# Kernel tuning notes

Measured on AMD Instinct MI355X. Metric: run time of the kernel, lower is better.

The kernel has to match this reference:

```python
import jax, jax.numpy as jnp
import numpy as np

BN_EPS = 1e-5


def setup_inputs() -> dict:
    key = jax.random.key(0)
    ks = jax.random.split(key, 7)
    B, C, N = 8, 512, 2048
    P = C // 2
    x = jax.random.normal(ks[0], (B, C, N), dtype=jnp.float32)
    # 1x1 conv weights (no bias), shape [out, in]
    Wg = jax.random.normal(ks[1], (P, C), dtype=jnp.float32) * (1.0 / np.sqrt(C))
    Wtheta = jax.random.normal(ks[2], (P, C), dtype=jnp.float32) * (1.0 / np.sqrt(C))
    Wphi = jax.random.normal(ks[3], (P, C), dtype=jnp.float32) * (1.0 / np.sqrt(C))
    Wz = jax.random.normal(ks[4], (C, P), dtype=jnp.float32) * (1.0 / np.sqrt(P))
    gamma = jnp.ones((C,), dtype=jnp.float32)
    beta = jnp.zeros((C,), dtype=jnp.float32)
    return {"x": x, "Wg": Wg, "Wtheta": Wtheta, "Wphi": Wphi, "Wz": Wz,
            "gamma": gamma, "beta": beta}


def reference(x, Wg, Wtheta, Wphi, Wz, gamma, beta):
    # x: [B, C, N]
    g = jnp.einsum('pc,bcn->bnp', Wg, x)        # [B, N, P]
    theta = jnp.einsum('pc,bcn->bnp', Wtheta, x)  # [B, N, P]
    phi = jnp.einsum('pc,bcn->bpn', Wphi, x)      # [B, P, N]
    f = jnp.einsum('bnp,bpm->bnm', theta, phi)    # [B, N, N] unscaled scores
    f = jax.nn.softmax(f, axis=-1)
    y = jnp.einsum('bnm,bmp->bpn', f, g)          # [B, P, N]
    z = jnp.einsum('cp,bpn->bcn', Wz, y)          # [B, C, N]
    # BatchNorm1d (training-mode batch stats over batch and length dims)
    mean = jnp.mean(z, axis=(0, 2), keepdims=True)
    var = jnp.mean((z - mean) ** 2, axis=(0, 2), keepdims=True)
    z_bn = (z - mean) / jnp.sqrt(var + BN_EPS)
    z_bn = z_bn * gamma[None, :, None] + beta[None, :, None]
    return z_bn + x
```

## Files before the change

### kernel.cpp

```cpp
#include <hip/hip_runtime.h>
#include <hip/hip_bf16.h>


typedef __attribute__((ext_vector_type(8))) short short8;
typedef __attribute__((ext_vector_type(4))) float floatx4;

__device__ __forceinline__ unsigned short f2bf(float v) {
    __hip_bfloat16 h = __float2bfloat16(v);
    return *(unsigned short*)&h;
}
__device__ __forceinline__ float bf2f(unsigned short u) {
    __hip_bfloat16 h;
    *(unsigned short*)&h = u;
    return __bfloat162float(h);
}

__global__ __launch_bounds__(256) void transpose_split(
    const float* __restrict__ X, unsigned short* __restrict__ Thi,
    unsigned short* __restrict__ Tlo, int R, int N)
{
    X   += (long)blockIdx.z * R * N;
    Thi += (long)blockIdx.z * N * R;
    Tlo += (long)blockIdx.z * N * R;
    __shared__ float s[32][33];
    const int tx = threadIdx.x & 31, ty = threadIdx.x >> 5;
    const int n0 = blockIdx.x * 32, r0 = blockIdx.y * 32;
#pragma unroll
    for (int r = 0; r < 4; ++r)
        s[ty + r * 8][tx] = X[(long)(r0 + ty + r * 8) * N + n0 + tx];
    __syncthreads();
#pragma unroll
    for (int r = 0; r < 4; ++r) {
        const int n = ty + r * 8;
        const float v = s[tx][n];
        const unsigned short hi = f2bf(v);
        const unsigned short lo = f2bf(v - bf2f(hi));
        Thi[(long)(n0 + n) * R + r0 + tx] = hi;
        Tlo[(long)(n0 + n) * R + r0 + tx] = lo;
    }
}

__global__ __launch_bounds__(256) void split_w2(
    const float* __restrict__ Wth, const float* __restrict__ Wph,
    unsigned short* __restrict__ Whi, unsigned short* __restrict__ Wlo, int PC)
{
    const int i = blockIdx.x * 256 + threadIdx.x;
    if (i < 2 * PC) {
        const float v = (i < PC) ? Wth[i] : Wph[i - PC];
        const unsigned short hi = f2bf(v);
        Whi[i] = hi;
        Wlo[i] = f2bf(v - bf2f(hi));
    }
}

__global__ __launch_bounds__(256) void cast_bf16(
    const float* __restrict__ X, unsigned short* __restrict__ Y)
{
    const long i = ((long)blockIdx.x * 256 + threadIdx.x) * 4;
    const float4 v = *(const float4*)&X[i];
    ushort4 o;
    o.x = f2bf(v.x); o.y = f2bf(v.y); o.z = f2bf(v.z); o.w = f2bf(v.w);
    *(ushort4*)&Y[i] = o;
}

#define BK 32

template <bool SPLIT, int OUTMODE, int FM, int FN>
__global__ __launch_bounds__(256) void mfma_gemm(
    const unsigned short* __restrict__ Ahi, const unsigned short* __restrict__ Alo,
    const unsigned short* __restrict__ Bhi, const unsigned short* __restrict__ Blo,
    void* __restrict__ Cout, void* __restrict__ Cout2,
    int K, int lda, int ldb, int ldc,
    long sA, long sB, long sC,
    float* __restrict__ S1, float* __restrict__ S2)
{
    constexpr int MTM = FM * 32, MTN = FN * 32;
    constexpr int SA = FM / 2, SB = FN / 2;

    Ahi += (long)blockIdx.z * sA;
    Bhi += (long)blockIdx.z * sB;
    if (SPLIT) { Alo += (long)blockIdx.z * sA; Blo += (long)blockIdx.z * sB; }
    float* Cf = (float*)Cout + (long)blockIdx.z * sC;
    unsigned short* Ch = (unsigned short*)Cout + (long)blockIdx.z * sC;
    unsigned short* Cl = (unsigned short*)Cout2 + (long)blockIdx.z * sC;

    __shared__ unsigned short AsH[MTM * BK], BsH[MTN * BK];
    __shared__ unsigned short AsL[SPLIT ? MTM * BK : 8], BsL[SPLIT ? MTN * BK : 8];

    const int tid = threadIdx.x;
    const int wid = tid >> 6, lane = tid & 63;
    const int wm = (wid >> 1) * (FM * 16), wn = (wid & 1) * (FN * 16);
    const int l15 = lane & 15, quad = lane >> 4;
    const int m0 = blockIdx.y * MTM, n0 = blockIdx.x * MTN;

    int arow[SA], acol[SA], brow[SB], bcol[SB];
#pragma unroll
    for (int t = 0; t < SA; ++t) {
        const int gid = t * 256 + tid;
        arow[t] = gid >> 2; acol[t] = (gid & 3) * 8;
    }
#pragma unroll
    for (int t = 0; t < SB; ++t) {
        const int gid = t * 256 + tid;
        brow[t] = gid >> 2; bcol[t] = (gid & 3) * 8;
    }

    short8 pa[SA], pb[SB], paL[SPLIT ? SA : 1], pbL[SPLIT ? SB : 1];

    auto loadTiles = [&](int k0) {
#pragma unroll
        for (int t = 0; t < SA; ++t) {
            const long o = (long)(m0 + arow[t]) * lda + k0 + acol[t];
            pa[t] = *(const short8*)&Ahi[o];
            if (SPLIT) paL[t] = *(const short8*)&Alo[o];
        }
#pragma unroll
        for (int t = 0; t < SB; ++t) {
            const long o = (long)(n0 + brow[t]) * ldb + k0 + bcol[t];
            pb[t] = *(const short8*)&Bhi[o];
            if (SPLIT) pbL[t] = *(const short8*)&Blo[o];
        }
    };
    auto writeTiles = [&]() {
#pragma unroll
        for (int t = 0; t < SA; ++t) {
            *(short8*)&AsH[arow[t] * BK + acol[t]] = pa[t];
            if (SPLIT) *(short8*)&AsL[arow[t] * BK + acol[t]] = paL[t];
        }
#pragma unroll
        for (int t = 0; t < SB; ++t) {
            *(short8*)&BsH[brow[t] * BK + bcol[t]] = pb[t];
            if (SPLIT) *(short8*)&BsL[brow[t] * BK + bcol[t]] = pbL[t];
        }
    };

    floatx4 acc[FM][FN];
#pragma unroll
    for (int i = 0; i < FM; ++i)
#pragma unroll
        for (int j = 0; j < FN; ++j) acc[i][j] = (floatx4){0.f, 0.f, 0.f, 0.f};

    const int iters = K / BK;
    loadTiles(0);
    writeTiles();
    __syncthreads();

    for (int it = 0; it < iters; ++it) {
        if (it + 1 < iters) loadTiles((it + 1) * BK);

        short8 ah[FM], bh[FN], al[SPLIT ? FM : 1], bl[SPLIT ? FN : 1];
#pragma unroll
        for (int i = 0; i < FM; ++i) {
            ah[i] = *(const short8*)&AsH[(wm + i * 16 + l15) * BK + quad * 8];
            if (SPLIT) al[i] = *(const short8*)&AsL[(wm + i * 16 + l15) * BK + quad * 8];
        }
#pragma unroll
        for (int j = 0; j < FN; ++j) {
            bh[j] = *(const short8*)&BsH[(wn + j * 16 + l15) * BK + quad * 8];
            if (SPLIT) bl[j] = *(const short8*)&BsL[(wn + j * 16 + l15) * BK + quad * 8];
        }
#pragma unroll
        for (int i = 0; i < FM; ++i)
#pragma unroll
            for (int j = 0; j < FN; ++j) {
                acc[i][j] = __builtin_amdgcn_mfma_f32_16x16x32_bf16(ah[i], bh[j], acc[i][j], 0, 0, 0);
                if (SPLIT) {
                    acc[i][j] = __builtin_amdgcn_mfma_f32_16x16x32_bf16(ah[i], bl[j], acc[i][j], 0, 0, 0);
                    acc[i][j] = __builtin_amdgcn_mfma_f32_16x16x32_bf16(al[i], bh[j], acc[i][j], 0, 0, 0);
                }
            }

        if (it + 1 < iters) {
            __syncthreads();
            writeTiles();
            __syncthreads();
        }
    }

#pragma unroll
    for (int i = 0; i < FM; ++i)
#pragma unroll
        for (int j = 0; j < FN; ++j) {
            const int m = m0 + wm + i * 16 + quad * 4;
            const int n = n0 + wn + j * 16 + l15;
#pragma unroll
            for (int r = 0; r < 4; ++r) {
                const float v = acc[i][j][r];
                const long idx = (long)(m + r) * ldc + n;
                if (OUTMODE == 0) {
                    Cf[idx] = v;
                } else if (OUTMODE == 1 || OUTMODE == 3) {
                    Ch[idx] = f2bf(v);
                } else {
                    const unsigned short hi = f2bf(v);
                    Ch[idx] = hi;
                    Cl[idx] = f2bf(v - bf2f(hi));
                }
            }
        }

    if (OUTMODE == 3) {
        const int slot = (blockIdx.z * gridDim.x + blockIdx.x) * 2 + (wn >> 6);
#pragma unroll
        for (int i = 0; i < FM; ++i)
#pragma unroll
            for (int r = 0; r < 4; ++r) {
                float s = 0.f, q = 0.f;
#pragma unroll
                for (int j = 0; j < FN; ++j) {
                    const float v = acc[i][j][r];
                    s += v; q += v * v;
                }
#pragma unroll
                for (int msk = 1; msk < 16; msk <<= 1) {
                    s += __shfl_xor(s, msk, 64);
                    q += __shfl_xor(q, msk, 64);
                }
                if (l15 == 0) {
                    const int row = m0 + wm + i * 16 + quad * 4 + r;
                    S1[(long)row * 256 + slot] = s;
                    S2[(long)row * 256 + slot] = q;
                }
            }
    }
}

#define FSTR 72
#define GSTR 72
#define PSTRP 136

__global__ __launch_bounds__(256) void fused_attn(
    const unsigned short* __restrict__ thphH,
    const unsigned short* __restrict__ thphL,
    const unsigned short* __restrict__ gbf,
    unsigned short* __restrict__ ybf)
{
    const int N = 2048, P = 256, P2 = 512;
    const int id = blockIdx.x;
    const int b  = id & 7;
    const int qt = id >> 3;
    const int q0 = qt * 64;

    const unsigned short* thB = thphH + (long)b * N * P2;
    const unsigned short* tlB = thphL + (long)b * N * P2;
    const unsigned short* gB  = gbf   + (long)b * P * N;
    unsigned short*       yB  = ybf   + (long)b * N * P;

    __shared__ unsigned short Fh[128 * FSTR], Fl[128 * FSTR];
    __shared__ unsigned short Gs[256 * GSTR];
    __shared__ unsigned short Pw[4][16 * PSTRP];

    const int tid = threadIdx.x;
    const int wid = tid >> 6, lane = tid & 63;
    const int l15 = lane & 15, quad = lane >> 4;

    short8 tHr[8], tLr[8];
    {
        const unsigned short* t1 = thB + (long)(q0 + wid * 16 + l15) * P2;
        const unsigned short* t2 = tlB + (long)(q0 + wid * 16 + l15) * P2;
#pragma unroll
        for (int kt = 0; kt < 8; ++kt) {
            tHr[kt] = *(const short8*)&t1[kt * 32 + quad * 8];
            tLr[kt] = *(const short8*)&t2[kt * 32 + quad * 8];
        }
    }

    float mrun[4], lrun[4];
#pragma unroll
    for (int r = 0; r < 4; ++r) { mrun[r] = -1e30f; lrun[r] = 0.f; }

    floatx4 oacc[16];
#pragma unroll
    for (int p = 0; p < 16; ++p) oacc[p] = (floatx4){0.f, 0.f, 0.f, 0.f};

    const int prow = tid >> 3, pc8 = (tid & 7) * 8;
    short8 pfH[4], pfL[4], pg[8];

    auto loadPhi = [&](int m0, int kc) {
#pragma unroll
        for (int s = 0; s < 4; ++s) {
            const long o = (long)(m0 + prow + s * 32) * P2 + P + kc * 64 + pc8;
            pfH[s] = *(const short8*)&thB[o];
            pfL[s] = *(const short8*)&tlB[o];
        }
    };
    auto writePhi = [&]() {
#pragma unroll
        for (int s = 0; s < 4; ++s) {
            *(short8*)&Fh[(prow + s * 32) * FSTR + pc8] = pfH[s];
            *(short8*)&Fl[(prow + s * 32) * FSTR + pc8] = pfL[s];
        }
    };
    auto loadG = [&](int m0, int mc) {
#pragma unroll
        for (int s = 0; s < 8; ++s)
            pg[s] = *(const short8*)&gB[(long)(prow + s * 32) * N + m0 + mc * 64 + pc8];
    };
    auto writeG = [&]() {
#pragma unroll
        for (int s = 0; s < 8; ++s)
            *(short8*)&Gs[(prow + s * 32) * GSTR + pc8] = pg[s];
    };

    for (int mt = 0; mt < 16; ++mt) {
        const int m0 = mt * 128;

        floatx4 sacc[8];
#pragma unroll
        for (int j = 0; j < 8; ++j) sacc[j] = (floatx4){0.f, 0.f, 0.f, 0.f};

        loadPhi(m0, 0);
        writePhi();
        __syncthreads();
#pragma unroll
        for (int kc = 0; kc < 4; ++kc) {
            if (kc < 3) loadPhi(m0, kc + 1);
#pragma unroll
            for (int ks = 0; ks < 2; ++ks) {
                const short8 aH = tHr[kc * 2 + ks];
                const short8 aL = tLr[kc * 2 + ks];
#pragma unroll
                for (int j = 0; j < 8; ++j) {
                    const int ro = (j * 16 + l15) * FSTR + ks * 32 + quad * 8;
                    const short8 bh = *(const short8*)&Fh[ro];
                    const short8 bl = *(const short8*)&Fl[ro];
                    sacc[j] = __builtin_amdgcn_mfma_f32_16x16x32_bf16(aH, bh, sacc[j], 0, 0, 0);
                    sacc[j] = __builtin_amdgcn_mfma_f32_16x16x32_bf16(aH, bl, sacc[j], 0, 0, 0);
                    sacc[j] = __builtin_amdgcn_mfma_f32_16x16x32_bf16(aL, bh, sacc[j], 0, 0, 0);
                }
            }
            if (kc < 3) {
                __syncthreads();
                writePhi();
                __syncthreads();
            }
        }

        float alpha[4];
#pragma unroll
        for (int r = 0; r < 4; ++r) {
            float v = sacc[0][r];
#pragma unroll
            for (int j = 1; j < 8; ++j) v = fmaxf(v, sacc[j][r]);
            v = fmaxf(v, __shfl_xor(v, 1, 64));
            v = fmaxf(v, __shfl_xor(v, 2, 64));
            v = fmaxf(v, __shfl_xor(v, 4, 64));
            v = fmaxf(v, __shfl_xor(v, 8, 64));
            const float mo = mrun[r];
            const float mn = fmaxf(mo, v);
            mrun[r] = mn;
            alpha[r] = __expf(mo - mn);
        }
        float lpart[4] = {0.f, 0.f, 0.f, 0.f};
#pragma unroll
        for (int j = 0; j < 8; ++j)
#pragma unroll
            for (int r = 0; r < 4; ++r) {
                const float p = __expf(sacc[j][r] - mrun[r]);
                Pw[wid][(quad * 4 + r) * PSTRP + j * 16 + l15] = f2bf(p);
                lpart[r] += p;
            }
#pragma unroll
        for (int r = 0; r < 4; ++r) {
            float s = lpart[r];
            s += __shfl_xor(s, 1, 64);
            s += __shfl_xor(s, 2, 64);
            s += __shfl_xor(s, 4, 64);
            s += __shfl_xor(s, 8, 64);
            lrun[r] = lrun[r] * alpha[r] + s;
        }
#pragma unroll
        for (int p = 0; p < 16; ++p)
#pragma unroll
            for (int r = 0; r < 4; ++r) oacc[p][r] *= alpha[r];

        loadG(m0, 0);
        writeG();
        __syncthreads();
#pragma unroll
        for (int mc = 0; mc < 2; ++mc) {
            if (mc == 0) loadG(m0, 1);
#pragma unroll
            for (int kk = 0; kk < 2; ++kk) {
                const short8 af = *(const short8*)&Pw[wid][l15 * PSTRP + mc * 64 + kk * 32 + quad * 8];
#pragma unroll
                for (int pj = 0; pj < 16; ++pj) {
                    const short8 bg = *(const short8*)&Gs[(pj * 16 + l15) * GSTR + kk * 32 + quad * 8];
                    oacc[pj] = __builtin_amdgcn_mfma_f32_16x16x32_bf16(af, bg, oacc[pj], 0, 0, 0);
                }
            }
            if (mc == 0) {
                __syncthreads();
                writeG();
                __syncthreads();
            }
        }
    }

    float linv[4];
#pragma unroll
    for (int r = 0; r < 4; ++r) linv[r] = 1.0f / lrun[r];
#pragma unroll
    for (int pj = 0; pj < 16; ++pj)
#pragma unroll
        for (int r = 0; r < 4; ++r) {
            const int row = q0 + wid * 16 + quad * 4 + r;
            const int col = pj * 16 + l15;
            yB[(long)row * P + col] = f2bf(oacc[pj][r] * linv[r]);
        }
}

__global__ __launch_bounds__(256) void bn_finalize(
    const float* __restrict__ p1, const float* __restrict__ p2,
    float* __restrict__ mean, float* __restrict__ rstd, float cnt)
{
    const int c = blockIdx.x, t = threadIdx.x;
    __shared__ float rs[256], rq[256];
    rs[t] = p1[(long)c * 256 + t];
    rq[t] = p2[(long)c * 256 + t];
    __syncthreads();
    for (int st = 128; st > 0; st >>= 1) {
        if (t < st) { rs[t] += rs[t + st]; rq[t] += rq[t + st]; }
        __syncthreads();
    }
    if (t == 0) {
        const float m = rs[0] / cnt;
        mean[c] = m;
        rstd[c] = rsqrtf(rq[0] / cnt - m * m + 1e-5f);
    }
}

__global__ __launch_bounds__(256) void bn_apply_bf(
    const unsigned short* __restrict__ z, const float* __restrict__ x,
    const float* __restrict__ mean, const float* __restrict__ rstd,
    const float* __restrict__ gamma, const float* __restrict__ beta,
    float* __restrict__ out, int C, int N)
{
    const long i = ((long)blockIdx.x * 256 + threadIdx.x) * 8;
    const int c = (int)((i / N) % C);
    const float mu = mean[c], rs = rstd[c], ga = gamma[c], be = beta[c];
    const ushort4 z0 = *(const ushort4*)&z[i];
    const ushort4 z1 = *(const ushort4*)&z[i + 4];
    const float4 x0 = *(const float4*)&x[i];
    const float4 x1 = *(const float4*)&x[i + 4];
    float4 o0, o1;
    o0.x = (bf2f(z0.x) - mu) * rs * ga + be + x0.x;
    o0.y = (bf2f(z0.y) - mu) * rs * ga + be + x0.y;
    o0.z = (bf2f(z0.z) - mu) * rs * ga + be + x0.z;
    o0.w = (bf2f(z0.w) - mu) * rs * ga + be + x0.w;
    o1.x = (bf2f(z1.x) - mu) * rs * ga + be + x1.x;
    o1.y = (bf2f(z1.y) - mu) * rs * ga + be + x1.y;
    o1.z = (bf2f(z1.z) - mu) * rs * ga + be + x1.z;
    o1.w = (bf2f(z1.w) - mu) * rs * ga + be + x1.w;
    *(float4*)&out[i] = o0;
    *(float4*)&out[i + 4] = o1;
}

extern "C" void kernel_launch(void* const* d_in, const int* in_sizes, int n_in,
                              void* d_out, int out_size, void* d_ws, size_t ws_size,
                              hipStream_t stream)
{
    const int B = 8, C = 512, N = 2048, P = 256;
    const float* x      = (const float*)d_in[0];
    const float* Wg     = (const float*)d_in[1];
    const float* Wtheta = (const float*)d_in[2];
    const float* Wphi   = (const float*)d_in[3];
    const float* Wz     = (const float*)d_in[4];
    const float* gamma  = (const float*)d_in[5];
    const float* beta   = (const float*)d_in[6];
    float* out = (float*)d_out;

    float* ws = (float*)d_ws;
    const long NCle = (long)N * C;
    const long NP   = (long)N * P;
    const long R0   = (long)B * NCle;
    unsigned short* xtH   = (unsigned short*)ws;
    unsigned short* xtL   = xtH + B * NCle;
    unsigned short* zbf   = (unsigned short*)ws;
    unsigned short* thphH = (unsigned short*)(ws + R0);
    unsigned short* thphL = thphH + B * NCle;
    unsigned short* gbf   = (unsigned short*)(ws + 2 * R0);
    unsigned short* fbf   = gbf + B * NP;
    unsigned short* ybf   = fbf + (long)B * N * N;
    unsigned short* W2H   = ybf + B * NP;
    unsigned short* W2L   = W2H + 2L * P * C;
    unsigned short* WgB   = W2L + 2L * P * C;
    unsigned short* WzB   = WgB + (long)P * C;
    float*          bnp1  = ws + R0;
    float*          bnp2  = bnp1 + (long)C * 256;
    float*          mean  = bnp2 + (long)C * 256;
    float*          rstd  = mean + C;

    const long sX = (long)C * N;
    const int  P2 = 2 * P;

    transpose_split<<<dim3(N / 32, C / 32, B), 256, 0, stream>>>(x, xtH, xtL, C, N);
    split_w2<<<(2 * P * C + 255) / 256, 256, 0, stream>>>(Wtheta, Wphi, W2H, W2L, P * C);
    cast_bf16<<<P * C / 1024, 256, 0, stream>>>(Wg, WgB);
    cast_bf16<<<P * C / 1024, 256, 0, stream>>>(Wz, WzB);

    mfma_gemm<true, 2, 4, 4><<<dim3(P2 / 128, N / 128, B), 256, 0, stream>>>(
        xtH, xtL, W2H, W2L, thphH, thphL, C, C, C, P2, NCle, 0, NCle, nullptr, nullptr);
    mfma_gemm<false, 1, 2, 4><<<dim3(N / 128, P / 64, B), 256, 0, stream>>>(
        WgB, WgB, xtH, xtH, gbf, gbf, C, C, C, N, 0, NCle, NP, nullptr, nullptr);

    fused_attn<<<dim3(256), 256, 0, stream>>>(thphH, thphL, gbf, ybf);

    mfma_gemm<false, 3, 4, 4><<<dim3(N / 128, C / 128, B), 256, 0, stream>>>(
        WzB, WzB, ybf, ybf, zbf, zbf, P, P, P, N, 0, NP, sX, bnp1, bnp2);

    bn_finalize<<<C, 256, 0, stream>>>(bnp1, bnp2, mean, rstd, (float)B * N);
    bn_apply_bf<<<(int)((B * sX) / 2048), 256, 0, stream>>>(zbf, x, mean, rstd, gamma, beta, out, C, N);
}
```

Baseline: 297.4 us.

## Split attention key range across two blocks and merge partial softmax results

The fused attention kernel now splits the key dimension into two halves, launching 512 blocks instead of 256. Each block writes unnormalized fp32 partial outputs plus running max and sum, and a new merge kernel rescales and combines them into the bf16 y tensor. This aims to fill more compute units on a GPU with many CUs, where 256 blocks underutilize the device. In exchange it adds fp32 partial-output traffic and an extra launch. The phi staging tile is also narrowed to 32 columns per chunk with a smaller LDS stride, which means more sync rounds per tile.

```diff
diff --git a/kernel.cpp b/kernel.cpp
--- a/kernel.cpp
+++ b/kernel.cpp
@@ -225,7 +225,7 @@
     }
 }
 
-#define FSTR 72
+#define FSTR4 40
 #define GSTR 72
 #define PSTRP 136
 
@@ -233,20 +233,26 @@
     const unsigned short* __restrict__ thphH,
     const unsigned short* __restrict__ thphL,
     const unsigned short* __restrict__ gbf,
-    unsigned short* __restrict__ ybf)
+    float* __restrict__ Opart,
+    float* __restrict__ Mpart,
+    float* __restrict__ Lpart)
 {
     const int N = 2048, P = 256, P2 = 512;
+    const long BN = 8L * 2048;
     const int id = blockIdx.x;
-    const int b  = id & 7;
-    const int qt = id >> 3;
+    const int b    = id & 7;
+    const int qt   = (id >> 3) & 31;
+    const int half = id >> 8;
     const int q0 = qt * 64;
 
     const unsigned short* thB = thphH + (long)b * N * P2;
     const unsigned short* tlB = thphL + (long)b * N * P2;
     const unsigned short* gB  = gbf   + (long)b * P * N;
-    unsigned short*       yB  = ybf   + (long)b * N * P;
-
-    __shared__ unsigned short Fh[128 * FSTR], Fl[128 * FSTR];
+    float* Oh = Opart + (long)half * BN * P;
+    float* Mh = Mpart + (long)half * BN;
+    float* Lh = Lpart + (long)half * BN;
+
+    __shared__ unsigned short Fh[128 * FSTR4], Fl[128 * FSTR4];
     __shared__ unsigned short Gs[256 * GSTR];
     __shared__ unsigned short Pw[4][16 * PSTRP];
 
@@ -273,36 +279,39 @@
 #pragma unroll
     for (int p = 0; p < 16; ++p) oacc[p] = (floatx4){0.f, 0.f, 0.f, 0.f};
 
-    const int prow = tid >> 3, pc8 = (tid & 7) * 8;
-    short8 pfH[4], pfL[4], pg[8];
+    short8 pfH[2], pfL[2], pg[8];
+    const int grow = tid >> 3, gc8 = (tid & 7) * 8;
 
     auto loadPhi = [&](int m0, int kc) {
 #pragma unroll
-        for (int s = 0; s < 4; ++s) {
-            const long o = (long)(m0 + prow + s * 32) * P2 + P + kc * 64 + pc8;
+        for (int s = 0; s < 2; ++s) {
+            const int gid = s * 256 + tid;
+            const long o = (long)(m0 + (gid >> 2)) * P2 + P + kc * 32 + (gid & 3) * 8;
             pfH[s] = *(const short8*)&thB[o];
             pfL[s] = *(const short8*)&tlB[o];
         }
     };
     auto writePhi = [&]() {
 #pragma unroll
-        for (int s = 0; s < 4; ++s) {
-            *(short8*)&Fh[(prow + s * 32) * FSTR + pc8] = pfH[s];
-            *(short8*)&Fl[(prow + s * 32) * FSTR + pc8] = pfL[s];
+        for (int s = 0; s < 2; ++s) {
+            const int gid = s * 256 + tid;
+            const int lo = (gid >> 2) * FSTR4 + (gid & 3) * 8;
+            *(short8*)&Fh[lo] = pfH[s];
+            *(short8*)&Fl[lo] = pfL[s];
         }
     };
     auto loadG = [&](int m0, int mc) {
 #pragma unroll
         for (int s = 0; s < 8; ++s)
-            pg[s] = *(const short8*)&gB[(long)(prow + s * 32) * N + m0 + mc * 64 + pc8];
+            pg[s] = *(const short8*)&gB[(long)(grow + s * 32) * N + m0 + mc * 64 + gc8];
     };
     auto writeG = [&]() {
 #pragma unroll
         for (int s = 0; s < 8; ++s)
-            *(short8*)&Gs[(prow + s * 32) * GSTR + pc8] = pg[s];
+            *(short8*)&Gs[(grow + s * 32) * GSTR + gc8] = pg[s];
     };
 
-    for (int mt = 0; mt < 16; ++mt) {
+    for (int mt = half * 8; mt < half * 8 + 8; ++mt) {
         const int m0 = mt * 128;
 
         floatx4 sacc[8];
@@ -313,23 +322,20 @@
         writePhi();
         __syncthreads();
 #pragma unroll
-        for (int kc = 0; kc < 4; ++kc) {
-            if (kc < 3) loadPhi(m0, kc + 1);
-#pragma unroll
-            for (int ks = 0; ks < 2; ++ks) {
-                const short8 aH = tHr[kc * 2 + ks];
-                const short8 aL = tLr[kc * 2 + ks];
-#pragma unroll
-                for (int j = 0; j < 8; ++j) {
-                    const int ro = (j * 16 + l15) * FSTR + ks * 32 + quad * 8;
-                    const short8 bh = *(const short8*)&Fh[ro];
-                    const short8 bl = *(const short8*)&Fl[ro];
-                    sacc[j] = __builtin_amdgcn_mfma_f32_16x16x32_bf16(aH, bh, sacc[j], 0, 0, 0);
-                    sacc[j] = __builtin_amdgcn_mfma_f32_16x16x32_bf16(aH, bl, sacc[j], 0, 0, 0);
-                    sacc[j] = __builtin_amdgcn_mfma_f32_16x16x32_bf16(aL, bh, sacc[j], 0, 0, 0);
-                }
-            }
-            if (kc < 3) {
+        for (int kc = 0; kc < 8; ++kc) {
+            if (kc < 7) loadPhi(m0, kc + 1);
+            const short8 aH = tHr[kc];
+            const short8 aL = tLr[kc];
+#pragma unroll
+            for (int j = 0; j < 8; ++j) {
+                const int ro = (j * 16 + l15) * FSTR4 + quad * 8;
+                const short8 bh = *(const short8*)&Fh[ro];
+                const short8 bl = *(const short8*)&Fl[ro];
+                sacc[j] = __builtin_amdgcn_mfma_f32_16x16x32_bf16(aH, bh, sacc[j], 0, 0, 0);
+                sacc[j] = __builtin_amdgcn_mfma_f32_16x16x32_bf16(aH, bl, sacc[j], 0, 0, 0);
+                sacc[j] = __builtin_amdgcn_mfma_f32_16x16x32_bf16(aL, bh, sacc[j], 0, 0, 0);
+            }
+            if (kc < 7) {
                 __syncthreads();
                 writePhi();
                 __syncthreads();
@@ -397,17 +403,47 @@
         }
     }
 
-    float linv[4];
-#pragma unroll
-    for (int r = 0; r < 4; ++r) linv[r] = 1.0f / lrun[r];
+    const long rbase = (long)b * N + q0 + wid * 16 + quad * 4;
 #pragma unroll
     for (int pj = 0; pj < 16; ++pj)
 #pragma unroll
+        for (int r = 0; r < 4; ++r)
+            Oh[(rbase + r) * P + pj * 16 + l15] = oacc[pj][r];
+    if (l15 == 0) {
+#pragma unroll
         for (int r = 0; r < 4; ++r) {
-            const int row = q0 + wid * 16 + quad * 4 + r;
-            const int col = pj * 16 + l15;
-            yB[(long)row * P + col] = f2bf(oacc[pj][r] * linv[r]);
-        }
+            Mh[rbase + r] = mrun[r];
+            Lh[rbase + r] = lrun[r];
+        }
+    }
+}
+
+__global__ __launch_bounds__(256) void merge_y(
+    const float* __restrict__ Opart, const float* __restrict__ Mpart,
+    const float* __restrict__ Lpart, unsigned short* __restrict__ ybf)
+{
+    const int P = 256;
+    const long BN = 8L * 2048;
+    const long row = (long)blockIdx.x * 8 + (threadIdx.x >> 5);
+    const int c0 = (threadIdx.x & 31) * 8;
+    const float m0 = Mpart[row], m1 = Mpart[BN + row];
+    const float mm = fmaxf(m0, m1);
+    const float w0 = __expf(m0 - mm), w1 = __expf(m1 - mm);
+    const float linv = 1.0f / (Lpart[row] * w0 + Lpart[BN + row] * w1);
+    const float* o0 = Opart + row * P + c0;
+    const float* o1 = Opart + BN * P + row * P + c0;
+    ushort4 outv[2];
+#pragma unroll
+    for (int h = 0; h < 2; ++h) {
+        const float4 a = *(const float4*)&o0[h * 4];
+        const float4 bq = *(const float4*)&o1[h * 4];
+        outv[h].x = f2bf((a.x * w0 + bq.x * w1) * linv);
+        outv[h].y = f2bf((a.y * w0 + bq.y * w1) * linv);
+        outv[h].z = f2bf((a.z * w0 + bq.z * w1) * linv);
+        outv[h].w = f2bf((a.w * w0 + bq.w * w1) * linv);
+    }
+    *(ushort4*)&ybf[row * P + c0] = outv[0];
+    *(ushort4*)&ybf[row * P + c0 + 4] = outv[1];
 }
 
 __global__ __launch_bounds__(256) void bn_finalize(
@@ -474,6 +510,7 @@
     const long NCle = (long)N * C;
     const long NP   = (long)N * P;
     const long R0   = (long)B * NCle;
+    const long BN   = (long)B * N;
     unsigned short* xtH   = (unsigned short*)ws;
     unsigned short* xtL   = xtH + B * NCle;
     unsigned short* zbf   = (unsigned short*)ws;
@@ -486,6 +523,9 @@
     unsigned short* W2L   = W2H + 2L * P * C;
     unsigned short* WgB   = W2L + 2L * P * C;
     unsigned short* WzB   = WgB + (long)P * C;
+    float*          Opart = (float*)fbf;
+    float*          Mpart = Opart + 2 * BN * (long)P;
+    float*          Lpart = Mpart + 2 * BN;
     float*          bnp1  = ws + R0;
     float*          bnp2  = bnp1 + (long)C * 256;
     float*          mean  = bnp2 + (long)C * 256;
@@ -504,7 +544,8 @@
     mfma_gemm<false, 1, 2, 4><<<dim3(N / 128, P / 64, B), 256, 0, stream>>>(
         WgB, WgB, xtH, xtH, gbf, gbf, C, C, C, N, 0, NCle, NP, nullptr, nullptr);
 
-    fused_attn<<<dim3(256), 256, 0, stream>>>(thphH, thphL, gbf, ybf);
+    fused_attn<<<dim3(512), 256, 0, stream>>>(thphH, thphL, gbf, Opart, Mpart, Lpart);
+    merge_y<<<dim3((int)(BN / 8)), 256, 0, stream>>>(Opart, Mpart, Lpart, ybf);
 
     mfma_gemm<false, 3, 4, 4><<<dim3(N / 128, C / 128, B), 256, 0, stream>>>(
         WzB, WzB, ybf, ybf, zbf, zbf, P, P, P, N, 0, NP, sX, bnp1, bnp2);
```

Result: slower. 329.2 us (+10.7%).
